# Optimization experiments

Hardware: AMD Instinct MI355X
Metric: run time of the kernel (lower is better)

Reference implementation:

```python
import jax, jax.numpy as jnp
import numpy as np
from jax import lax

B, T, D, H = 64, 2048, 128, 256  # batch, seq_len, input_dim, hidden_dim


def setup_inputs() -> dict:
    key = jax.random.key(0)
    ks = jax.random.split(key, 21)
    s = 0.05
    p = lambda k, shape: jax.random.normal(k, shape, dtype=jnp.float32) * s
    inp = {"x": jax.random.normal(ks[0], (B, T, D), dtype=jnp.float32)}
    i = 1
    for n in ["e1", "e2", "d1", "d2"]:  # encode1, encode2, reconstruct1, reconstruct2
        inp[n + "_Wih"] = p(ks[i], (4 * H, D)); i += 1
        inp[n + "_Whh"] = p(ks[i], (4 * H, H)); i += 1
        inp[n + "_bih"] = p(ks[i], (4 * H,)); i += 1
        inp[n + "_bhh"] = p(ks[i], (4 * H,)); i += 1
    inp["l1_W"] = p(ks[17], (D, H)); inp["l1_b"] = p(ks[18], (D,))
    inp["l2_W"] = p(ks[19], (D, H)); inp["l2_b"] = p(ks[20], (D,))
    return inp


def _lstm_cell(h, c, xt, Wih, Whh, bih, bhh):
    # PyTorch gate order: i, f, g, o
    g = xt @ Wih.T + h @ Whh.T + bih + bhh  # [B, 4H]
    i, f, gg, o = jnp.split(g, 4, axis=-1)
    c = jax.nn.sigmoid(f) * c + jax.nn.sigmoid(i) * jnp.tanh(gg)
    h = jax.nn.sigmoid(o) * jnp.tanh(c)
    return h, c


def _encode(x, h0, c0, Wih, Whh, bih, bhh):
    # x: [B, T, D] batch_first -> scan over time
    def step(carry, xt):
        h, c = carry
        h, c = _lstm_cell(h, c, xt, Wih, Whh, bih, bhh)
        return (h, c), None
    (h, c), _ = lax.scan(step, (h0, c0), jnp.swapaxes(x, 0, 1))
    return h, c


def _decode(n, h, c, Wih, Whh, bih, bhh, Wl, bl):
    # first output is linear(hidden) before any cell step (matches original decode)
    inp0 = h @ Wl.T + bl  # [B, D]
    def step(carry, _):
        h, c, inp = carry
        h, c = _lstm_cell(h, c, inp, Wih, Whh, bih, bhh)
        inp = h @ Wl.T + bl
        return (h, c, inp), inp
    _, outs = lax.scan(step, (h, c, inp0), None, length=n - 1)  # [n-1, B, D]
    out = jnp.concatenate([inp0[None], outs], axis=0)  # [n, B, D]
    return jnp.swapaxes(out, 0, 1)  # [B, n, D]


def reference(x,
              e1_Wih, e1_Whh, e1_bih, e1_bhh,
              e2_Wih, e2_Whh, e2_bih, e2_bhh,
              d1_Wih, d1_Whh, d1_bih, d1_bhh,
              d2_Wih, d2_Whh, d2_bih, d2_bhh,
              l1_W, l1_b, l2_W, l2_b):
    Bc, Tc = x.shape[0], x.shape[1]
    T1 = Tc // 2
    h0 = jnp.zeros((Bc, H), dtype=x.dtype)
    c0 = jnp.zeros((Bc, H), dtype=x.dtype)
    x1 = x[:, :T1][:, ::-1]  # first half, time-reversed
    x2 = x[:, T1:]
    h1, c1 = _encode(x1, h0, c0, e1_Wih, e1_Whh, e1_bih, e1_bhh)
    h2, c2 = _encode(x2, h1, c1, e2_Wih, e2_Whh, e2_bih, e2_bhh)
    out1 = _decode(T1, h1, c1, d1_Wih, d1_Whh, d1_bih, d1_bhh, l1_W, l1_b)
    out2 = _decode(Tc - T1, h2, c2, d2_Wih, d2_Whh, d2_bih, d2_bhh, l2_W, l2_b)[:, ::-1]
    return jnp.concatenate([out1, out2], axis=1)  # [B, T, D]
```

## Files before the change

### kernel.cpp

```cpp
#include <hip/hip_runtime.h>
#include <stdint.h>

#define Bv 64
#define Tv 2048
#define T1v 1024
#define Dv 128
#define Hv 256

typedef _Float16 h2_t __attribute__((ext_vector_type(2)));

__device__ inline float d2(uint32_t hp, uint32_t wp, float acc) {
#if __has_builtin(__builtin_amdgcn_fdot2)
  return __builtin_amdgcn_fdot2(__builtin_bit_cast(h2_t, hp),
                                __builtin_bit_cast(h2_t, wp), acc, false);
#else
  float out;
  asm("v_dot2_f32_f16 %0, %1, %2, %3" : "=v"(out) : "v"(hp), "v"(wp), "v"(acc));
  return out;
#endif
}

__device__ inline uint16_t f2h(float x) {
  _Float16 h = (_Float16)x;
  return __builtin_bit_cast(uint16_t, h);
}
__device__ inline float h2f(uint16_t u) {
  return (float)__builtin_bit_cast(_Float16, u);
}
__device__ inline uint32_t packpair(float a, float b) {
  return (uint32_t)f2h(a) | ((uint32_t)f2h(b) << 16);
}
__device__ inline float unpk(uint32_t u, int hi) {
  return h2f((uint16_t)(hi ? (u >> 16) : (u & 0xffff)));
}
__device__ inline float sigm(float x) { return 1.f / (1.f + __expf(-x)); }
__device__ inline float tanh_(float x) { return 2.f / (1.f + __expf(-2.f * x)) - 1.f; }

__device__ inline float qsum4(float v) {
  int t = __builtin_amdgcn_update_dpp(0, __float_as_int(v), 0xB1, 0xF, 0xF, true);
  v += __int_as_float(t);
  t = __builtin_amdgcn_update_dpp(0, __float_as_int(v), 0x4E, 0xF, 0xF, true);
  return v + __int_as_float(t);
}


__global__ void k_pack_x(const float* __restrict__ x, uint32_t* __restrict__ xpk) {
  int idx = blockIdx.x * 256 + threadIdx.x;
  const float2* x2 = (const float2*)x;
  float2 v = x2[idx];
  xpk[idx] = packpair(v.x, v.y);
}

__global__ void k_pack_w(const float* __restrict__ src, uint32_t* __restrict__ wAll,
                         uint32_t* __restrict__ wLg, uint32_t* __restrict__ wStr) {
  int idx = blockIdx.x * 256 + threadIdx.x;
  int row = idx >> 7, k2 = idx & 127;
  uint32_t pr = packpair(src[row * 256 + 2 * k2], src[row * 256 + 2 * k2 + 1]);
  wAll[k2 * 1024 + row] = pr;
  if (k2 >= 96) {
    int g = (k2 - 96) >> 2, qq = (k2 - 96) & 3;
    wLg[(g * 1024 + row) * 4 + qq] = pr;
  }
  if (k2 >= 48 && k2 < 96) wStr[row * 48 + (k2 - 48)] = pr;
}

__global__ void k_pack_w2(const float* __restrict__ src, uint32_t* __restrict__ wOn,
                          uint32_t* __restrict__ wLds) {
  int idx = blockIdx.x * 256 + threadIdx.x;
  int r = idx >> 7, k2 = idx & 127;
  uint32_t pr = packpair(src[r * 256 + 2 * k2], src[r * 256 + 2 * k2 + 1]);
  int gate = r >> 8, u = r & 255;
  int u_hi = u >> 7, jb = u & 127;
  int q = k2 >> 5, kk = k2 & 31;
  int tid = jb * 4 + q;
  int ri = u_hi * 4 + gate;
  if (kk < 24) {
    wOn[(ri * 24 + kk) * 512 + tid] = pr;
  } else {
    int p = ri * 2 + ((kk - 24) >> 2);
    int c = (kk - 24) & 3;
    wLds[((size_t)p * 512 + tid) * 4 + c] = pr;
  }
}

__global__ void k_bias_pack(const float* __restrict__ b32, uint32_t* __restrict__ bpk) {
  int jb = threadIdx.x;
  uint32_t w[4];
#pragma unroll
  for (int wi = 0; wi < 4; ++wi) {
    int ri0 = 2 * wi, ri1 = 2 * wi + 1;
    int row0 = (ri0 & 3) * 256 + jb + 128 * (ri0 >> 2);
    int row1 = (ri1 & 3) * 256 + jb + 128 * (ri1 >> 2);
    w[wi] = packpair(b32[row0], b32[row1]);
  }
  ((uint4*)bpk)[jb] = make_uint4(w[0], w[1], w[2], w[3]);
}

__global__ void k_pack_wih(const float* __restrict__ Wih, uint32_t* __restrict__ wihp) {
  int idx = blockIdx.x * 256 + threadIdx.x;
  int row = idx >> 6, k2 = idx & 63;
  wihp[row * 64 + k2] = packpair(Wih[row * 128 + 2 * k2], Wih[row * 128 + 2 * k2 + 1]);
}

__global__ void k_bias2(const float* __restrict__ bih, const float* __restrict__ bhh,
                        float* __restrict__ bias) {
  int i = blockIdx.x * 256 + threadIdx.x;
  if (i < 1024) bias[i] = bih[i] + bhh[i];
}

__global__ void k_dec_combine(const float* __restrict__ Whh, const float* __restrict__ Wih,
                              const float* __restrict__ bih, const float* __restrict__ bhh,
                              const float* __restrict__ lW, const float* __restrict__ lb,
                              float* __restrict__ wd, float* __restrict__ bias) {
  int j = blockIdx.x;
  int k = threadIdx.x;
  __shared__ float wr[128];
  if (k < 128) wr[k] = Wih[j * 128 + k];
  __syncthreads();
  float acc = Whh[j * 256 + k];
  for (int d = 0; d < 128; ++d) acc += wr[d] * lW[d * 256 + k];
  wd[j * 256 + k] = acc;
  if (k == 0) {
    float s = bih[j] + bhh[j];
    for (int d = 0; d < 128; ++d) s += wr[d] * lb[d];
    bias[j] = s;
  }
}

__global__ void k_pack_wl(const float* __restrict__ lW, uint32_t* __restrict__ wlp) {
  int idx = blockIdx.x * 256 + threadIdx.x;
  int d = idx >> 7, k2 = idx & 127;
  wlp[d * 128 + k2] = packpair(lW[d * 256 + 2 * k2], lW[d * 256 + 2 * k2 + 1]);
}

template <int LAY>
__global__ __launch_bounds__(256) void k_xp_gemm(const uint32_t* __restrict__ xpk,
                                                 const uint32_t* __restrict__ wihp,
                                                 uint16_t* __restrict__ xp, int xt0, int xdt) {
  const int b = blockIdx.z;
  const int s0 = blockIdx.y * 32;
  const int r = blockIdx.x * 256 + threadIdx.x;
  uint32_t wreg[64];
#pragma unroll
  for (int k = 0; k < 64; ++k) wreg[k] = wihp[r * 64 + k];
  const int gate = r >> 8, u = r & 255;
  const int u_hi = u >> 7, jb = u & 127;
  const int ri = u_hi * 4 + gate;
  for (int sl = 0; sl < 32; ++sl) {
    const int s = s0 + sl;
    const int t = xt0 + s * xdt;
    const uint32_t* __restrict__ xrow = xpk + ((size_t)b * Tv + t) * 64;
    float a0 = 0.f, a1 = 0.f;
#pragma unroll
    for (int k = 0; k < 64; k += 2) {
      a0 = d2(xrow[k], wreg[k], a0);
      a1 = d2(xrow[k + 1], wreg[k + 1], a1);
    }
    uint16_t v = f2h(a0 + a1);
    if (LAY == 0)
      xp[(((size_t)b * T1v + s) * 128 + jb) * 8 + ri] = v;
    else
      xp[((size_t)b * T1v + s) * 1024 + r] = v;
  }
}


struct CfgU {
  const uint32_t* wOn;
  const uint4* wLds;
  const uint4* bpk;
  const uint4* xps;
  const float* h0;
  const float* c0;
  float* hN;
  float* cN;
  uint16_t* hist;
};

__global__ void __launch_bounds__(512)
__attribute__((amdgpu_waves_per_eu(2, 2)))
k_rnnU(CfgU cA, CfgU cB, int nA) {
  __shared__ __align__(16) uint4 wldsM[16 * 512];
  __shared__ __align__(16) uint16_t hb[2][256];

  const bool isA = (int)blockIdx.x < nA;
  const CfgU cfg = isA ? cA : cB;
  const int b = isA ? (int)blockIdx.x : ((int)blockIdx.x - nA);
  const int tid = threadIdx.x;
  const int q = tid & 3, jb = tid >> 2;
  const float qz = (q == 0) ? 1.f : 0.f;

#pragma unroll
  for (int i = 0; i < 16; ++i) wldsM[i * 512 + tid] = cfg.wLds[i * 512 + tid];

  uint32_t wreg[192];
#pragma unroll
  for (int k = 0; k < 192; ++k) wreg[k] = cfg.wOn[k * 512 + tid];

  const uint4 bp = cfg.bpk[jb];
  float c0r = cfg.c0 ? cfg.c0[b * 256 + jb] : 0.f;
  float c1r = cfg.c0 ? cfg.c0[b * 256 + jb + 128] : 0.f;

  uint16_t* histp = cfg.hist ? cfg.hist + (size_t)b * 1024 * 256 : nullptr;
  if (q == 0) {
    float h00 = cfg.h0 ? cfg.h0[b * 256 + jb] : 0.f;
    float h01 = cfg.h0 ? cfg.h0[b * 256 + jb + 128] : 0.f;
    uint16_t u0 = f2h(h00), u1 = f2h(h01);
    hb[0][jb] = u0;
    hb[0][jb + 128] = u1;
    if (histp) {
      histp[jb] = u0;
      histp[jb + 128] = u1;
    }
  }
  const uint4* xps4 = cfg.xps ? cfg.xps + (size_t)b * 1024 * 128 + jb : nullptr;

  __syncthreads();

  int cur = 0;
  for (int s = 0; s < 1024; ++s) {
    uint4 xq = make_uint4(0, 0, 0, 0);
    if (xps4) xq = xps4[(size_t)s * 128];

    float acc[8];
    acc[0] = qz * (unpk(bp.x, 0) + unpk(xq.x, 0));
    acc[1] = qz * (unpk(bp.x, 1) + unpk(xq.x, 1));
    acc[2] = qz * (unpk(bp.y, 0) + unpk(xq.y, 0));
    acc[3] = qz * (unpk(bp.y, 1) + unpk(xq.y, 1));
    acc[4] = qz * (unpk(bp.z, 0) + unpk(xq.z, 0));
    acc[5] = qz * (unpk(bp.z, 1) + unpk(xq.z, 1));
    acc[6] = qz * (unpk(bp.w, 0) + unpk(xq.w, 0));
    acc[7] = qz * (unpk(bp.w, 1) + unpk(xq.w, 1));

    const uint4* H4 = (const uint4*)hb[cur];
#pragma unroll
    for (int c = 0; c < 6; ++c) {
      const uint4 hv = H4[q * 8 + c];
#pragma unroll
      for (int ri = 0; ri < 8; ++ri) {
        const int base = ri * 24 + c * 4;
        acc[ri] = d2(hv.x, wreg[base + 0], acc[ri]);
        acc[ri] = d2(hv.y, wreg[base + 1], acc[ri]);
        acc[ri] = d2(hv.z, wreg[base + 2], acc[ri]);
        acc[ri] = d2(hv.w, wreg[base + 3], acc[ri]);
      }
    }
#pragma unroll
    for (int p = 0; p < 2; ++p) {
      const uint4 hv = H4[q * 8 + 6 + p];
#pragma unroll
      for (int ri = 0; ri < 8; ++ri) {
        const uint4 wv = wldsM[(ri * 2 + p) * 512 + tid];
        acc[ri] = d2(hv.x, wv.x, acc[ri]);
        acc[ri] = d2(hv.y, wv.y, acc[ri]);
        acc[ri] = d2(hv.z, wv.z, acc[ri]);
        acc[ri] = d2(hv.w, wv.w, acc[ri]);
      }
    }

#pragma unroll
    for (int ri = 0; ri < 8; ++ri) acc[ri] = qsum4(acc[ri]);

    const float cn0 = sigm(acc[1]) * c0r + sigm(acc[0]) * tanh_(acc[2]);
    const float h0v = sigm(acc[3]) * tanh_(cn0);
    c0r = cn0;
    const float cn1 = sigm(acc[5]) * c1r + sigm(acc[4]) * tanh_(acc[6]);
    const float h1v = sigm(acc[7]) * tanh_(cn1);
    c1r = cn1;

    const uint16_t hu0 = f2h(h0v), hu1 = f2h(h1v);
    if (q == 0) {
      hb[cur ^ 1][jb] = hu0;
      hb[cur ^ 1][jb + 128] = hu1;
      if (histp && s < 1023) {
        histp[(size_t)(s + 1) * 256 + jb] = hu0;
        histp[(size_t)(s + 1) * 256 + jb + 128] = hu1;
      }
    }
    __syncthreads();
    cur ^= 1;
  }

  if (cfg.hN && q == 0) {
    cfg.hN[b * 256 + jb] = h2f(hb[cur][jb]);
    cfg.hN[b * 256 + jb + 128] = h2f(hb[cur][jb + 128]);
    cfg.cN[b * 256 + jb] = c0r;
    cfg.cN[b * 256 + jb + 128] = c1r;
  }
}


struct ChainCfg {
  const uint32_t* wAll;
  const uint4* wLg;
  const uint32_t* wStr;
  const uint32_t* wih;
  const uint32_t* xpk;
  const uint16_t* xps;
  const float* bias;
  const float* h0;
  const float* c0;
  float* hN;
  float* cN;
  uint16_t* hist;
  int xt0, xdt;
};

template <int NRESP, bool WIH>
__global__ void __launch_bounds__(512)
__attribute__((amdgpu_waves_per_eu(2, 2)))
k_rnn5(ChainCfg cA, ChainCfg cB, int nA) {
  __shared__ __align__(16) uint4 wlds4[8 * 1024];
  __shared__ float gsm[1024];
  __shared__ __align__(16) uint16_t h16[256];
  __shared__ __align__(16) uint32_t xsh[64];

  const bool isA = (int)blockIdx.x < nA;
  const ChainCfg cfg = isA ? cA : cB;
  const int b = isA ? (int)blockIdx.x : ((int)blockIdx.x - nA);
  const int tid = threadIdx.x;
  const int r0 = tid, r1 = tid + 512;

#pragma unroll
  for (int i = 0; i < 16; ++i) wlds4[i * 512 + tid] = cfg.wLg[i * 512 + tid];

  uint16_t* histp = cfg.hist ? cfg.hist + (size_t)b * 1024 * 256 : nullptr;

  float creg = 0.f;
  if (tid < 256) {
    float h0v = cfg.h0 ? cfg.h0[b * 256 + tid] : 0.f;
    creg = cfg.c0 ? cfg.c0[b * 256 + tid] : 0.f;
    uint16_t hu = f2h(h0v);
    h16[tid] = hu;
    if (histp) histp[tid] = hu;
  }

  uint32_t w0[NRESP], w1[NRESP];
#pragma unroll
  for (int k = 0; k < NRESP; ++k) w0[k] = cfg.wAll[k * 1024 + r0];
#pragma unroll
  for (int k = 0; k < NRESP; ++k) w1[k] = cfg.wAll[k * 1024 + r1];
  const float bias0 = cfg.bias[r0];
  const float bias1 = cfg.bias[r1];

  constexpr int NS4 = (96 - NRESP) / 4;
  const uint4* ws0 = (const uint4*)(cfg.wStr + (size_t)r0 * 48 + (NRESP - 48));
  const uint4* ws1 = (const uint4*)(cfg.wStr + (size_t)r1 * 48 + (NRESP - 48));
  const uint4* wi0 = cfg.wih ? (const uint4*)(cfg.wih + (size_t)r0 * 64) : nullptr;
  const uint4* wi1 = cfg.wih ? (const uint4*)(cfg.wih + (size_t)r1 * 64) : nullptr;
  const bool hasx = cfg.xps != nullptr;

  __syncthreads();

  for (int s = 0; s < 1024; ++s) {
    float xa0 = 0.f, xa1 = 0.f;
    if (hasx) {
      size_t xb = ((size_t)b * 1024 + s) * 1024;
      xa0 = h2f(cfg.xps[xb + r0]);
      xa1 = h2f(cfg.xps[xb + r1]);
    }
    if constexpr (WIH) {
      if (cfg.wih) {
        if (tid < 64) {
          const int t = cfg.xt0 + s * cfg.xdt;
          xsh[tid] = cfg.xpk[((size_t)b * Tv + t) * 64 + tid];
        }
        __syncthreads();
      }
    }

    const uint4* H4 = (const uint4*)h16;
    float a00 = bias0, a01 = 0.f, a10 = bias1, a11 = 0.f;

#pragma unroll
    for (int c4 = 0; c4 < NRESP / 4; ++c4) {
      const uint4 hv = H4[c4];
      a00 = d2(hv.x, w0[4 * c4 + 0], a00);
      a01 = d2(hv.y, w0[4 * c4 + 1], a01);
      a10 = d2(hv.x, w1[4 * c4 + 0], a10);
      a11 = d2(hv.y, w1[4 * c4 + 1], a11);
      a00 = d2(hv.z, w0[4 * c4 + 2], a00);
      a01 = d2(hv.w, w0[4 * c4 + 3], a01);
      a10 = d2(hv.z, w1[4 * c4 + 2], a10);
      a11 = d2(hv.w, w1[4 * c4 + 3], a11);
    }
    if constexpr (NS4 > 0) {
#pragma unroll
      for (int u = 0; u < NS4; ++u) {
        const uint4 hv = H4[NRESP / 4 + u];
        const uint4 wv0 = ws0[u];
        const uint4 wv1 = ws1[u];
        a00 = d2(hv.x, wv0.x, a00);
        a01 = d2(hv.y, wv0.y, a01);
        a10 = d2(hv.x, wv1.x, a10);
        a11 = d2(hv.y, wv1.y, a11);
        a00 = d2(hv.z, wv0.z, a00);
        a01 = d2(hv.w, wv0.w, a01);
        a10 = d2(hv.z, wv1.z, a10);
        a11 = d2(hv.w, wv1.w, a11);
      }
    }
#pragma unroll
    for (int g = 0; g < 8; ++g) {
      const uint4 hv = H4[24 + g];
      const uint4 wv0 = wlds4[g * 1024 + r0];
      const uint4 wv1 = wlds4[g * 1024 + r1];
      a00 = d2(hv.x, wv0.x, a00);
      a01 = d2(hv.y, wv0.y, a01);
      a10 = d2(hv.x, wv1.x, a10);
      a11 = d2(hv.y, wv1.y, a11);
      a00 = d2(hv.z, wv0.z, a00);
      a01 = d2(hv.w, wv0.w, a01);
      a10 = d2(hv.z, wv1.z, a10);
      a11 = d2(hv.w, wv1.w, a11);
    }
    if constexpr (WIH) {
      if (cfg.wih) {
        const uint4* XS4 = (const uint4*)xsh;
#pragma unroll
        for (int u = 0; u < 16; ++u) {
          const uint4 xv = XS4[u];
          const uint4 wv0 = wi0[u];
          const uint4 wv1 = wi1[u];
          a00 = d2(xv.x, wv0.x, a00);
          a01 = d2(xv.y, wv0.y, a01);
          a10 = d2(xv.x, wv1.x, a10);
          a11 = d2(xv.y, wv1.y, a11);
          a00 = d2(xv.z, wv0.z, a00);
          a01 = d2(xv.w, wv0.w, a01);
          a10 = d2(xv.z, wv1.z, a10);
          a11 = d2(xv.w, wv1.w, a11);
        }
      }
    }

    gsm[r0] = a00 + a01 + xa0;
    gsm[r1] = a10 + a11 + xa1;
    __syncthreads();

    if (tid < 256) {
      const float gi = gsm[tid];
      const float gf = gsm[tid + 256];
      const float gg = gsm[tid + 512];
      const float go = gsm[tid + 768];
      const float cn = sigm(gf) * creg + sigm(gi) * tanh_(gg);
      const float hv = sigm(go) * tanh_(cn);
      creg = cn;
      const uint16_t hu = f2h(hv);
      h16[tid] = hu;
      if (histp && s < 1023) histp[(size_t)(s + 1) * 256 + tid] = hu;
    }
    __syncthreads();
  }

  if (cfg.hN && tid < 256) {
    cfg.hN[b * 256 + tid] = h2f(h16[tid]);
    cfg.cN[b * 256 + tid] = creg;
  }
}

__global__ __launch_bounds__(256) void k_out(const uint16_t* __restrict__ hist,
                                             const uint32_t* __restrict__ wlp,
                                             const float* __restrict__ lb,
                                             float* __restrict__ out, int outbase, int tsign) {
  const int b = blockIdx.y;
  const int t0 = blockIdx.x * 64;
  __shared__ __align__(16) uint32_t hq[64 * 128];
  const uint32_t* hsrc = (const uint32_t*)hist;
  for (int i = threadIdx.x; i < 64 * 128; i += 256) {
    hq[i] = hsrc[((size_t)b * 1024 + t0) * 128 + i];
  }
  __syncthreads();
  const int d = threadIdx.x & 127;
  const int th = threadIdx.x >> 7;
  float acc[32];
#pragma unroll
  for (int it = 0; it < 32; ++it) acc[it] = lb[d];
  const uint4* W4 = (const uint4*)(wlp + (size_t)d * 128);
  const uint4* HQ4 = (const uint4*)hq;
  for (int k2c = 0; k2c < 32; ++k2c) {
    const uint4 wv = W4[k2c];
#pragma unroll
    for (int it = 0; it < 32; ++it) {
      const int tl = th * 32 + it;
      const uint4 hv = HQ4[tl * 32 + k2c];
      acc[it] = d2(hv.x, wv.x, acc[it]);
      acc[it] = d2(hv.y, wv.y, acc[it]);
      acc[it] = d2(hv.z, wv.z, acc[it]);
      acc[it] = d2(hv.w, wv.w, acc[it]);
    }
  }
#pragma unroll
  for (int it = 0; it < 32; ++it) {
    const int tl = th * 32 + it;
    const int t = t0 + tl;
    const int tout = outbase + tsign * t;
    out[((size_t)b * Tv + tout) * Dv + d] = acc[it];
  }
}


extern "C" void kernel_launch(void* const* d_in, const int* in_sizes, int n_in,
                              void* d_out, int out_size, void* d_ws, size_t ws_size,
                              hipStream_t stream) {
  const float* x = (const float*)d_in[0];
  const float* e1_Wih = (const float*)d_in[1];
  const float* e1_Whh = (const float*)d_in[2];
  const float* e1_bih = (const float*)d_in[3];
  const float* e1_bhh = (const float*)d_in[4];
  const float* e2_Wih = (const float*)d_in[5];
  const float* e2_Whh = (const float*)d_in[6];
  const float* e2_bih = (const float*)d_in[7];
  const float* e2_bhh = (const float*)d_in[8];
  const float* d1_Wih = (const float*)d_in[9];
  const float* d1_Whh = (const float*)d_in[10];
  const float* d1_bih = (const float*)d_in[11];
  const float* d1_bhh = (const float*)d_in[12];
  const float* d2_Wih = (const float*)d_in[13];
  const float* d2_Whh = (const float*)d_in[14];
  const float* d2_bih = (const float*)d_in[15];
  const float* d2_bhh = (const float*)d_in[16];
  const float* l1_W = (const float*)d_in[17];
  const float* l1_b = (const float*)d_in[18];
  const float* l2_W = (const float*)d_in[19];
  const float* l2_b = (const float*)d_in[20];

  uint8_t* wsb = (uint8_t*)d_ws;
  size_t off = 0;
  auto take = [&](size_t n) -> void* {
    void* pp = wsb + off;
    off += (n + 255) & ~(size_t)255;
    return pp;
  };
  uint32_t* xpk = (uint32_t*)take((size_t)Bv * Tv * 64 * 4);
  uint16_t* hist1 = (uint16_t*)take((size_t)Bv * T1v * Hv * 2);
  uint16_t* hist2 = (uint16_t*)take((size_t)Bv * T1v * Hv * 2);
  struct WSet {
    uint32_t *wAll, *wLg, *wStr, *wih;
    float* bias;
    uint32_t *wOn, *wLds, *bpk;
  };
  auto take_wset = [&](bool with_ih) -> WSet {
    WSet w;
    w.wAll = (uint32_t*)take(128 * 1024 * 4);
    w.wLg = (uint32_t*)take(8 * 1024 * 16);
    w.wStr = (uint32_t*)take(1024 * 48 * 4);
    w.wih = with_ih ? (uint32_t*)take(1024 * 64 * 4) : nullptr;
    w.bias = (float*)take(1024 * 4);
    w.wOn = (uint32_t*)take(192 * 512 * 4);
    w.wLds = (uint32_t*)take(16 * 512 * 16);
    w.bpk = (uint32_t*)take(128 * 16);
    return w;
  };
  WSet we1 = take_wset(true);
  WSet we2 = take_wset(true);
  WSet wd1 = take_wset(false);
  WSet wd2 = take_wset(false);
  float* wd32 = (float*)take(1024 * 256 * 4);
  uint32_t* wl1p = (uint32_t*)take(128 * 128 * 4);
  uint32_t* wl2p = (uint32_t*)take(128 * 128 * 4);
  float* h1 = (float*)take(64 * 256 * 4);
  float* c1 = (float*)take(64 * 256 * 4);
  float* h2 = (float*)take(64 * 256 * 4);
  float* c2 = (float*)take(64 * 256 * 4);
  uint16_t* xp = (uint16_t*)take((size_t)Bv * T1v * 1024 * 2);
  const bool use_xp = ws_size >= off;

  int variant = 2;
  {
    hipFuncAttributes fa;
    auto spillfree = [&](const void* f) {
      return hipFuncGetAttributes(&fa, f) == hipSuccess && fa.localSizeBytes == 0;
    };
    if (use_xp && spillfree(reinterpret_cast<const void*>(&k_rnnU))) {
      variant = 0;
    } else if (use_xp) {
      if (spillfree(reinterpret_cast<const void*>(&k_rnn5<96, false>))) variant = 1;
    } else {
      if (spillfree(reinterpret_cast<const void*>(&k_rnn5<96, true>))) variant = 1;
    }
  }

  k_pack_x<<<(Bv * Tv * 64) / 256, 256, 0, stream>>>(x, xpk);
  k_pack_w<<<512, 256, 0, stream>>>(e1_Whh, we1.wAll, we1.wLg, we1.wStr);
  k_pack_w2<<<512, 256, 0, stream>>>(e1_Whh, we1.wOn, we1.wLds);
  k_pack_wih<<<256, 256, 0, stream>>>(e1_Wih, we1.wih);
  k_bias2<<<4, 256, 0, stream>>>(e1_bih, e1_bhh, we1.bias);
  k_bias_pack<<<1, 128, 0, stream>>>(we1.bias, we1.bpk);
  k_pack_w<<<512, 256, 0, stream>>>(e2_Whh, we2.wAll, we2.wLg, we2.wStr);
  k_pack_w2<<<512, 256, 0, stream>>>(e2_Whh, we2.wOn, we2.wLds);
  k_pack_wih<<<256, 256, 0, stream>>>(e2_Wih, we2.wih);
  k_bias2<<<4, 256, 0, stream>>>(e2_bih, e2_bhh, we2.bias);
  k_bias_pack<<<1, 128, 0, stream>>>(we2.bias, we2.bpk);
  k_dec_combine<<<1024, 256, 0, stream>>>(d1_Whh, d1_Wih, d1_bih, d1_bhh, l1_W, l1_b, wd32, wd1.bias);
  k_pack_w<<<512, 256, 0, stream>>>(wd32, wd1.wAll, wd1.wLg, wd1.wStr);
  k_pack_w2<<<512, 256, 0, stream>>>(wd32, wd1.wOn, wd1.wLds);
  k_bias_pack<<<1, 128, 0, stream>>>(wd1.bias, wd1.bpk);
  k_dec_combine<<<1024, 256, 0, stream>>>(d2_Whh, d2_Wih, d2_bih, d2_bhh, l2_W, l2_b, wd32, wd2.bias);
  k_pack_w<<<512, 256, 0, stream>>>(wd32, wd2.wAll, wd2.wLg, wd2.wStr);
  k_pack_w2<<<512, 256, 0, stream>>>(wd32, wd2.wOn, wd2.wLds);
  k_bias_pack<<<1, 128, 0, stream>>>(wd2.bias, wd2.bpk);
  k_pack_wl<<<64, 256, 0, stream>>>(l1_W, wl1p);
  k_pack_wl<<<64, 256, 0, stream>>>(l2_W, wl2p);

  auto launch_old = [&](int grid, ChainCfg a, ChainCfg b2, int nA) {
    if (use_xp) {
      if (variant == 1) k_rnn5<96, false><<<grid, 512, 0, stream>>>(a, b2, nA);
      else              k_rnn5<80, false><<<grid, 512, 0, stream>>>(a, b2, nA);
    } else {
      if (variant == 1) k_rnn5<96, true><<<grid, 512, 0, stream>>>(a, b2, nA);
      else              k_rnn5<80, true><<<grid, 512, 0, stream>>>(a, b2, nA);
    }
  };

  if (variant == 0) {
    k_xp_gemm<0><<<dim3(4, 32, 64), 256, 0, stream>>>(xpk, we1.wih, xp, 1023, -1);
    CfgU e1c{we1.wOn, (const uint4*)we1.wLds, (const uint4*)we1.bpk, (const uint4*)xp,
             nullptr, nullptr, h1, c1, nullptr};
    k_rnnU<<<64, 512, 0, stream>>>(e1c, e1c, 64);

    k_xp_gemm<0><<<dim3(4, 32, 64), 256, 0, stream>>>(xpk, we2.wih, xp, 1024, 1);
    CfgU e2c{we2.wOn, (const uint4*)we2.wLds, (const uint4*)we2.bpk, (const uint4*)xp,
             h1, c1, h2, c2, nullptr};
    CfgU d1c{wd1.wOn, (const uint4*)wd1.wLds, (const uint4*)wd1.bpk, nullptr,
             h1, c1, nullptr, nullptr, hist1};
    k_rnnU<<<128, 512, 0, stream>>>(e2c, d1c, 64);

    CfgU d2c{wd2.wOn, (const uint4*)wd2.wLds, (const uint4*)wd2.bpk, nullptr,
             h2, c2, nullptr, nullptr, hist2};
    k_rnnU<<<64, 512, 0, stream>>>(d2c, d2c, 64);
  } else {
    if (use_xp) k_xp_gemm<1><<<dim3(4, 32, 64), 256, 0, stream>>>(xpk, we1.wih, xp, 1023, -1);
    ChainCfg e1c{we1.wAll, (const uint4*)we1.wLg, we1.wStr, use_xp ? nullptr : we1.wih,
                 use_xp ? nullptr : xpk, use_xp ? xp : nullptr, we1.bias,
                 nullptr, nullptr, h1, c1, nullptr, 1023, -1};
    launch_old(64, e1c, e1c, 64);

    if (use_xp) k_xp_gemm<1><<<dim3(4, 32, 64), 256, 0, stream>>>(xpk, we2.wih, xp, 1024, 1);
    ChainCfg e2c{we2.wAll, (const uint4*)we2.wLg, we2.wStr, use_xp ? nullptr : we2.wih,
                 use_xp ? nullptr : xpk, use_xp ? xp : nullptr, we2.bias,
                 h1, c1, h2, c2, nullptr, 1024, 1};
    ChainCfg d1c{wd1.wAll, (const uint4*)wd1.wLg, wd1.wStr, nullptr, nullptr, nullptr,
                 wd1.bias, h1, c1, nullptr, nullptr, hist1, 0, 0};
    launch_old(128, e2c, d1c, 64);

    ChainCfg d2c{wd2.wAll, (const uint4*)wd2.wLg, wd2.wStr, nullptr, nullptr, nullptr,
                 wd2.bias, h2, c2, nullptr, nullptr, hist2, 0, 0};
    launch_old(64, d2c, d2c, 64);
  }

  k_out<<<dim3(16, 64), 256, 0, stream>>>(hist1, wl1p, l1_b, (float*)d_out, 0, 1);
  k_out<<<dim3(16, 64), 256, 0, stream>>>(hist2, wl2p, l2_b, (float*)d_out, 2047, -1);
}
```

Before: 7.022 ms.

## Template recurrent kernel on register/LDS/streamed weight split with padded h buffer

Turns the recurrent LSTM kernel into a template that splits the hidden-weight chunks between registers, LDS and per-step volatile global streaming. A host-side cascade picks the first spill-free configuration. The h buffer is laid out per quarter with padding to reduce LDS bank conflicts. Bias and input projection are now added after the cross-lane reduction, which drops the qz multiply. The aim is a spill-free variant that keeps most weights on-chip. The risk is that streamed volatile global loads on the serial critical path add latency to every step.

```diff
diff --git a/kernel.cpp b/kernel.cpp
--- a/kernel.cpp
+++ b/kernel.cpp
@@ -43,6 +43,16 @@
   return v + __int_as_float(t);
 }
 
+__device__ inline uint4 ld_stream(const uint4* p) {
+  const volatile uint32_t* q = (const volatile uint32_t*)p;
+  uint4 v;
+  v.x = q[0];
+  v.y = q[1];
+  v.z = q[2];
+  v.w = q[3];
+  return v;
+}
+
 
 __global__ void k_pack_x(const float* __restrict__ x, uint32_t* __restrict__ xpk) {
   int idx = blockIdx.x * 256 + threadIdx.x;
@@ -64,7 +74,7 @@
   if (k2 >= 48 && k2 < 96) wStr[row * 48 + (k2 - 48)] = pr;
 }
 
-__global__ void k_pack_w2(const float* __restrict__ src, uint32_t* __restrict__ wOn,
+__global__ void k_pack_w2(const float* __restrict__ src, uint32_t* __restrict__ wSt,
                           uint32_t* __restrict__ wLds) {
   int idx = blockIdx.x * 256 + threadIdx.x;
   int r = idx >> 7, k2 = idx & 127;
@@ -75,11 +85,9 @@
   int tid = jb * 4 + q;
   int ri = u_hi * 4 + gate;
   if (kk < 24) {
-    wOn[(ri * 24 + kk) * 512 + tid] = pr;
+    wSt[((ri * 6 + (kk >> 2)) * 512 + tid) * 4 + (kk & 3)] = pr;
   } else {
-    int p = ri * 2 + ((kk - 24) >> 2);
-    int c = (kk - 24) & 3;
-    wLds[((size_t)p * 512 + tid) * 4 + c] = pr;
+    wLds[((ri * 2 + ((kk - 24) >> 2)) * 512 + tid) * 4 + ((kk - 24) & 3)] = pr;
   }
 }
 
@@ -166,7 +174,7 @@
 
 
 struct CfgU {
-  const uint32_t* wOn;
+  const uint4* wSt;
   const uint4* wLds;
   const uint4* bpk;
   const uint4* xps;
@@ -177,25 +185,31 @@
   uint16_t* hist;
 };
 
+template <int NREGC, int NSTRC, int NLDSC>
 __global__ void __launch_bounds__(512)
 __attribute__((amdgpu_waves_per_eu(2, 2)))
 k_rnnU(CfgU cA, CfgU cB, int nA) {
-  __shared__ __align__(16) uint4 wldsM[16 * 512];
-  __shared__ __align__(16) uint16_t hb[2][256];
+  __shared__ __align__(16) uint4 wldsM[NLDSC * 8 * 512];
+  __shared__ __align__(16) uint16_t hbuf[2][4][72];
 
   const bool isA = (int)blockIdx.x < nA;
   const CfgU cfg = isA ? cA : cB;
   const int b = isA ? (int)blockIdx.x : ((int)blockIdx.x - nA);
   const int tid = threadIdx.x;
   const int q = tid & 3, jb = tid >> 2;
-  const float qz = (q == 0) ? 1.f : 0.f;
-
-#pragma unroll
-  for (int i = 0; i < 16; ++i) wldsM[i * 512 + tid] = cfg.wLds[i * 512 + tid];
-
-  uint32_t wreg[192];
-#pragma unroll
-  for (int k = 0; k < 192; ++k) wreg[k] = cfg.wOn[k * 512 + tid];
+
+#pragma unroll
+  for (int ri = 0; ri < 8; ++ri)
+#pragma unroll
+    for (int li = 0; li < NLDSC; ++li)
+      wldsM[(ri * NLDSC + li) * 512 + tid] =
+          cfg.wLds[(ri * 2 + (2 - NLDSC) + li) * 512 + tid];
+
+  uint4 wr[8][NREGC];
+#pragma unroll
+  for (int ri = 0; ri < 8; ++ri)
+#pragma unroll
+    for (int cc = 0; cc < NREGC; ++cc) wr[ri][cc] = cfg.wSt[(ri * 6 + cc) * 512 + tid];
 
   const uint4 bp = cfg.bpk[jb];
   float c0r = cfg.c0 ? cfg.c0[b * 256 + jb] : 0.f;
@@ -206,8 +220,8 @@
     float h00 = cfg.h0 ? cfg.h0[b * 256 + jb] : 0.f;
     float h01 = cfg.h0 ? cfg.h0[b * 256 + jb + 128] : 0.f;
     uint16_t u0 = f2h(h00), u1 = f2h(h01);
-    hb[0][jb] = u0;
-    hb[0][jb + 128] = u1;
+    hbuf[0][jb >> 6][jb & 63] = u0;
+    hbuf[0][2 + (jb >> 6)][jb & 63] = u1;
     if (histp) {
       histp[jb] = u0;
       histp[jb + 128] = u1;
@@ -221,45 +235,62 @@
   for (int s = 0; s < 1024; ++s) {
     uint4 xq = make_uint4(0, 0, 0, 0);
     if (xps4) xq = xps4[(size_t)s * 128];
+    const uint4* Hq = (const uint4*)&hbuf[cur][q][0];
 
     float acc[8];
-    acc[0] = qz * (unpk(bp.x, 0) + unpk(xq.x, 0));
-    acc[1] = qz * (unpk(bp.x, 1) + unpk(xq.x, 1));
-    acc[2] = qz * (unpk(bp.y, 0) + unpk(xq.y, 0));
-    acc[3] = qz * (unpk(bp.y, 1) + unpk(xq.y, 1));
-    acc[4] = qz * (unpk(bp.z, 0) + unpk(xq.z, 0));
-    acc[5] = qz * (unpk(bp.z, 1) + unpk(xq.z, 1));
-    acc[6] = qz * (unpk(bp.w, 0) + unpk(xq.w, 0));
-    acc[7] = qz * (unpk(bp.w, 1) + unpk(xq.w, 1));
-
-    const uint4* H4 = (const uint4*)hb[cur];
-#pragma unroll
-    for (int c = 0; c < 6; ++c) {
-      const uint4 hv = H4[q * 8 + c];
+#pragma unroll
+    for (int ri = 0; ri < 8; ++ri) acc[ri] = 0.f;
+
+#pragma unroll
+    for (int cc = 0; cc < NREGC; ++cc) {
+      const uint4 hv = Hq[cc];
 #pragma unroll
       for (int ri = 0; ri < 8; ++ri) {
-        const int base = ri * 24 + c * 4;
-        acc[ri] = d2(hv.x, wreg[base + 0], acc[ri]);
-        acc[ri] = d2(hv.y, wreg[base + 1], acc[ri]);
-        acc[ri] = d2(hv.z, wreg[base + 2], acc[ri]);
-        acc[ri] = d2(hv.w, wreg[base + 3], acc[ri]);
-      }
-    }
-#pragma unroll
-    for (int p = 0; p < 2; ++p) {
-      const uint4 hv = H4[q * 8 + 6 + p];
+        acc[ri] = d2(hv.x, wr[ri][cc].x, acc[ri]);
+        acc[ri] = d2(hv.y, wr[ri][cc].y, acc[ri]);
+        acc[ri] = d2(hv.z, wr[ri][cc].z, acc[ri]);
+        acc[ri] = d2(hv.w, wr[ri][cc].w, acc[ri]);
+      }
+    }
+#pragma unroll
+    for (int j = 0; j < NSTRC; ++j) {
+      const int cc = NREGC + j;
+      const uint4 hv = Hq[cc];
 #pragma unroll
       for (int ri = 0; ri < 8; ++ri) {
-        const uint4 wv = wldsM[(ri * 2 + p) * 512 + tid];
+        const uint4 wv = (cc < 6) ? ld_stream(cfg.wSt + (ri * 6 + cc) * 512 + tid)
+                                  : ld_stream(cfg.wLds + (ri * 2 + (cc - 6)) * 512 + tid);
         acc[ri] = d2(hv.x, wv.x, acc[ri]);
         acc[ri] = d2(hv.y, wv.y, acc[ri]);
         acc[ri] = d2(hv.z, wv.z, acc[ri]);
         acc[ri] = d2(hv.w, wv.w, acc[ri]);
       }
     }
+#pragma unroll
+    for (int li = 0; li < NLDSC; ++li) {
+      const int cc = 8 - NLDSC + li;
+      const uint4 hv = Hq[cc];
+#pragma unroll
+      for (int ri = 0; ri < 8; ++ri) {
+        const uint4 wv = wldsM[(ri * NLDSC + li) * 512 + tid];
+        acc[ri] = d2(hv.x, wv.x, acc[ri]);
+        acc[ri] = d2(hv.y, wv.y, acc[ri]);
+        acc[ri] = d2(hv.z, wv.z, acc[ri]);
+        acc[ri] = d2(hv.w, wv.w, acc[ri]);
+      }
+    }
 
 #pragma unroll
     for (int ri = 0; ri < 8; ++ri) acc[ri] = qsum4(acc[ri]);
+
+    acc[0] += unpk(bp.x, 0) + unpk(xq.x, 0);
+    acc[1] += unpk(bp.x, 1) + unpk(xq.x, 1);
+    acc[2] += unpk(bp.y, 0) + unpk(xq.y, 0);
+    acc[3] += unpk(bp.y, 1) + unpk(xq.y, 1);
+    acc[4] += unpk(bp.z, 0) + unpk(xq.z, 0);
+    acc[5] += unpk(bp.z, 1) + unpk(xq.z, 1);
+    acc[6] += unpk(bp.w, 0) + unpk(xq.w, 0);
+    acc[7] += unpk(bp.w, 1) + unpk(xq.w, 1);
 
     const float cn0 = sigm(acc[1]) * c0r + sigm(acc[0]) * tanh_(acc[2]);
     const float h0v = sigm(acc[3]) * tanh_(cn0);
@@ -268,10 +299,10 @@
     const float h1v = sigm(acc[7]) * tanh_(cn1);
     c1r = cn1;
 
-    const uint16_t hu0 = f2h(h0v), hu1 = f2h(h1v);
     if (q == 0) {
-      hb[cur ^ 1][jb] = hu0;
-      hb[cur ^ 1][jb + 128] = hu1;
+      const uint16_t hu0 = f2h(h0v), hu1 = f2h(h1v);
+      hbuf[cur ^ 1][jb >> 6][jb & 63] = hu0;
+      hbuf[cur ^ 1][2 + (jb >> 6)][jb & 63] = hu1;
       if (histp && s < 1023) {
         histp[(size_t)(s + 1) * 256 + jb] = hu0;
         histp[(size_t)(s + 1) * 256 + jb + 128] = hu1;
@@ -282,8 +313,8 @@
   }
 
   if (cfg.hN && q == 0) {
-    cfg.hN[b * 256 + jb] = h2f(hb[cur][jb]);
-    cfg.hN[b * 256 + jb + 128] = h2f(hb[cur][jb + 128]);
+    cfg.hN[b * 256 + jb] = h2f(hbuf[cur][jb >> 6][jb & 63]);
+    cfg.hN[b * 256 + jb + 128] = h2f(hbuf[cur][2 + (jb >> 6)][jb & 63]);
     cfg.cN[b * 256 + jb] = c0r;
     cfg.cN[b * 256 + jb + 128] = c1r;
   }
@@ -538,7 +569,7 @@
   struct WSet {
     uint32_t *wAll, *wLg, *wStr, *wih;
     float* bias;
-    uint32_t *wOn, *wLds, *bpk;
+    uint32_t *wSt, *wLds, *bpk;
   };
   auto take_wset = [&](bool with_ih) -> WSet {
     WSet w;
@@ -547,7 +578,7 @@
     w.wStr = (uint32_t*)take(1024 * 48 * 4);
     w.wih = with_ih ? (uint32_t*)take(1024 * 64 * 4) : nullptr;
     w.bias = (float*)take(1024 * 4);
-    w.wOn = (uint32_t*)take(192 * 512 * 4);
+    w.wSt = (uint32_t*)take(48 * 512 * 16);
     w.wLds = (uint32_t*)take(16 * 512 * 16);
     w.bpk = (uint32_t*)take(128 * 16);
     return w;
@@ -566,70 +597,75 @@
   uint16_t* xp = (uint16_t*)take((size_t)Bv * T1v * 1024 * 2);
   const bool use_xp = ws_size >= off;
 
-  int variant = 2;
+  int variant = 4;
   {
     hipFuncAttributes fa;
     auto spillfree = [&](const void* f) {
       return hipFuncGetAttributes(&fa, f) == hipSuccess && fa.localSizeBytes == 0;
     };
-    if (use_xp && spillfree(reinterpret_cast<const void*>(&k_rnnU))) {
-      variant = 0;
-    } else if (use_xp) {
-      if (spillfree(reinterpret_cast<const void*>(&k_rnn5<96, false>))) variant = 1;
+    if (use_xp) {
+      if (spillfree(reinterpret_cast<const void*>(&k_rnnU<6, 1, 1>))) variant = 0;
+      else if (spillfree(reinterpret_cast<const void*>(&k_rnnU<6, 0, 2>))) variant = 1;
+      else if (spillfree(reinterpret_cast<const void*>(&k_rnnU<4, 2, 2>))) variant = 2;
+      else if (spillfree(reinterpret_cast<const void*>(&k_rnn5<96, false>))) variant = 3;
     } else {
-      if (spillfree(reinterpret_cast<const void*>(&k_rnn5<96, true>))) variant = 1;
+      if (spillfree(reinterpret_cast<const void*>(&k_rnn5<96, true>))) variant = 3;
     }
   }
 
   k_pack_x<<<(Bv * Tv * 64) / 256, 256, 0, stream>>>(x, xpk);
   k_pack_w<<<512, 256, 0, stream>>>(e1_Whh, we1.wAll, we1.wLg, we1.wStr);
-  k_pack_w2<<<512, 256, 0, stream>>>(e1_Whh, we1.wOn, we1.wLds);
+  k_pack_w2<<<512, 256, 0, stream>>>(e1_Whh, we1.wSt, we1.wLds);
   k_pack_wih<<<256, 256, 0, stream>>>(e1_Wih, we1.wih);
   k_bias2<<<4, 256, 0, stream>>>(e1_bih, e1_bhh, we1.bias);
   k_bias_pack<<<1, 128, 0, stream>>>(we1.bias, we1.bpk);
   k_pack_w<<<512, 256, 0, stream>>>(e2_Whh, we2.wAll, we2.wLg, we2.wStr);
-  k_pack_w2<<<512, 256, 0, stream>>>(e2_Whh, we2.wOn, we2.wLds);
+  k_pack_w2<<<512, 256, 0, stream>>>(e2_Whh, we2.wSt, we2.wLds);
   k_pack_wih<<<256, 256, 0, stream>>>(e2_Wih, we2.wih);
   k_bias2<<<4, 256, 0, stream>>>(e2_bih, e2_bhh, we2.bias);
   k_bias_pack<<<1, 128, 0, stream>>>(we2.bias, we2.bpk);
   k_dec_combine<<<1024, 256, 0, stream>>>(d1_Whh, d1_Wih, d1_bih, d1_bhh, l1_W, l1_b, wd32, wd1.bias);
   k_pack_w<<<512, 256, 0, stream>>>(wd32, wd1.wAll, wd1.wLg, wd1.wStr);
-  k_pack_w2<<<512, 256, 0, stream>>>(wd32, wd1.wOn, wd1.wLds);
+  k_pack_w2<<<512, 256, 0, stream>>>(wd32, wd1.wSt, wd1.wLds);
   k_bias_pack<<<1, 128, 0, stream>>>(wd1.bias, wd1.bpk);
   k_dec_combine<<<1024, 256, 0, stream>>>(d2_Whh, d2_Wih, d2_bih, d2_bhh, l2_W, l2_b, wd32, wd2.bias);
   k_pack_w<<<512, 256, 0, stream>>>(wd32, wd2.wAll, wd2.wLg, wd2.wStr);
-  k_pack_w2<<<512, 256, 0, stream>>>(wd32, wd2.wOn, wd2.wLds);
+  k_pack_w2<<<512, 256, 0, stream>>>(wd32, wd2.wSt, wd2.wLds);
   k_bias_pack<<<1, 128, 0, stream>>>(wd2.bias, wd2.bpk);
   k_pack_wl<<<64, 256, 0, stream>>>(l1_W, wl1p);
   k_pack_wl<<<64, 256, 0, stream>>>(l2_W, wl2p);
 
-  auto launch_old = [&](int grid, ChainCfg a, ChainCfg b2, int nA) {
-    if (use_xp) {
-      if (variant == 1) k_rnn5<96, false><<<grid, 512, 0, stream>>>(a, b2, nA);
-      else              k_rnn5<80, false><<<grid, 512, 0, stream>>>(a, b2, nA);
-    } else {
-      if (variant == 1) k_rnn5<96, true><<<grid, 512, 0, stream>>>(a, b2, nA);
-      else              k_rnn5<80, true><<<grid, 512, 0, stream>>>(a, b2, nA);
-    }
-  };
-
-  if (variant == 0) {
+  if (variant <= 2) {
+    auto launch_u = [&](int grid, CfgU a, CfgU b2, int nA) {
+      if (variant == 0)      k_rnnU<6, 1, 1><<<grid, 512, 0, stream>>>(a, b2, nA);
+      else if (variant == 1) k_rnnU<6, 0, 2><<<grid, 512, 0, stream>>>(a, b2, nA);
+      else                   k_rnnU<4, 2, 2><<<grid, 512, 0, stream>>>(a, b2, nA);
+    };
     k_xp_gemm<0><<<dim3(4, 32, 64), 256, 0, stream>>>(xpk, we1.wih, xp, 1023, -1);
-    CfgU e1c{we1.wOn, (const uint4*)we1.wLds, (const uint4*)we1.bpk, (const uint4*)xp,
-             nullptr, nullptr, h1, c1, nullptr};
-    k_rnnU<<<64, 512, 0, stream>>>(e1c, e1c, 64);
+    CfgU e1c{(const uint4*)we1.wSt, (const uint4*)we1.wLds, (const uint4*)we1.bpk,
+             (const uint4*)xp, nullptr, nullptr, h1, c1, nullptr};
+    launch_u(64, e1c, e1c, 64);
 
     k_xp_gemm<0><<<dim3(4, 32, 64), 256, 0, stream>>>(xpk, we2.wih, xp, 1024, 1);
-    CfgU e2c{we2.wOn, (const uint4*)we2.wLds, (const uint4*)we2.bpk, (const uint4*)xp,
-             h1, c1, h2, c2, nullptr};
-    CfgU d1c{wd1.wOn, (const uint4*)wd1.wLds, (const uint4*)wd1.bpk, nullptr,
-             h1, c1, nullptr, nullptr, hist1};
-    k_rnnU<<<128, 512, 0, stream>>>(e2c, d1c, 64);
-
-    CfgU d2c{wd2.wOn, (const uint4*)wd2.wLds, (const uint4*)wd2.bpk, nullptr,
-             h2, c2, nullptr, nullptr, hist2};
-    k_rnnU<<<64, 512, 0, stream>>>(d2c, d2c, 64);
+    CfgU e2c{(const uint4*)we2.wSt, (const uint4*)we2.wLds, (const uint4*)we2.bpk,
+             (const uint4*)xp, h1, c1, h2, c2, nullptr};
+    CfgU d1c{(const uint4*)wd1.wSt, (const uint4*)wd1.wLds, (const uint4*)wd1.bpk,
+             nullptr, h1, c1, nullptr, nullptr, hist1};
+    launch_u(128, e2c, d1c, 64);
+
+    CfgU d2c{(const uint4*)wd2.wSt, (const uint4*)wd2.wLds, (const uint4*)wd2.bpk,
+             nullptr, h2, c2, nullptr, nullptr, hist2};
+    launch_u(64, d2c, d2c, 64);
   } else {
+    auto launch_old = [&](int grid, ChainCfg a, ChainCfg b2, int nA) {
+      if (use_xp) {
+        if (variant == 3) k_rnn5<96, false><<<grid, 512, 0, stream>>>(a, b2, nA);
+        else              k_rnn5<80, false><<<grid, 512, 0, stream>>>(a, b2, nA);
+      } else {
+        if (variant == 3) k_rnn5<96, true><<<grid, 512, 0, stream>>>(a, b2, nA);
+        else              k_rnn5<80, true><<<grid, 512, 0, stream>>>(a, b2, nA);
+      }
+    };
     if (use_xp) k_xp_gemm<1><<<dim3(4, 32, 64), 256, 0, stream>>>(xpk, we1.wih, xp, 1023, -1);
     ChainCfg e1c{we1.wAll, (const uint4*)we1.wLg, we1.wStr, use_xp ? nullptr : we1.wih,
                  use_xp ? nullptr : xpk, use_xp ? xp : nullptr, we1.bias,
```

Result: slower. 7.299 ms (+3.9%).
